# Kernel optimization log

Hardware: AMD Instinct MI355X
Metric: run time of the kernel (lower is better)

The kernel has to match this reference:

```python
import jax, jax.numpy as jnp
import numpy as np

EMBED_DIM = 1024
NUM_HEADS = 16
HEAD_DIM = EMBED_DIM // NUM_HEADS
TGT_LEN = 1024
SRC_LEN = 1024
BSZ = 4


def setup_inputs() -> dict:
    key = jax.random.key(0)
    ks = jax.random.split(key, 7)
    query = jax.random.normal(ks[0], (TGT_LEN, BSZ, EMBED_DIM), dtype=jnp.float32)
    key_t = jax.random.normal(ks[1], (SRC_LEN, BSZ, EMBED_DIM), dtype=jnp.float32)
    # hard 0/1 multiplicative mask applied post-softmax
    hard_attention = jax.random.randint(ks[2], (BSZ, TGT_LEN, SRC_LEN), 0, 2).astype(jnp.float32)
    # xavier_uniform_ on [3E, E]
    limit = float(np.sqrt(6.0 / (3 * EMBED_DIM + EMBED_DIM)))
    in_proj_weight = jax.random.uniform(ks[3], (3 * EMBED_DIM, EMBED_DIM), dtype=jnp.float32,
                                        minval=-limit, maxval=limit)
    in_proj_bias = jnp.zeros((3 * EMBED_DIM,), dtype=jnp.float32)
    limit_o = float(np.sqrt(1.0 / EMBED_DIM))
    out_proj_weight = jax.random.uniform(ks[4], (EMBED_DIM, EMBED_DIM), dtype=jnp.float32,
                                         minval=-limit_o, maxval=limit_o)
    out_proj_bias = jnp.zeros((EMBED_DIM,), dtype=jnp.float32)
    return {
        "query": query,
        "key": key_t,
        "hard_attention": hard_attention,
        "in_proj_weight": in_proj_weight,
        "in_proj_bias": in_proj_bias,
        "out_proj_weight": out_proj_weight,
        "out_proj_bias": out_proj_bias,
    }


def reference(query, key, hard_attention, in_proj_weight, in_proj_bias,
              out_proj_weight, out_proj_bias):
    tgt_len, bsz, embed_dim = query.shape
    src_len = key.shape[0]
    h, hd = NUM_HEADS, embed_dim // NUM_HEADS
    scaling = float(hd) ** -0.5

    # QKV projections (F.linear uses y = x @ W.T + b)
    wq = in_proj_weight[:embed_dim]
    wkv = in_proj_weight[embed_dim:]
    bq = in_proj_bias[:embed_dim]
    bkv = in_proj_bias[embed_dim:]
    q = jnp.einsum('tbe,fe->tbf', query, wq) + bq          # [T,B,E]
    kv = jnp.einsum('sbe,fe->sbf', key, wkv) + bkv          # [S,B,2E]
    k, v = jnp.split(kv, 2, axis=-1)

    q = (q * scaling).reshape(tgt_len, bsz, h, hd).transpose(1, 2, 0, 3)  # [B,H,T,D]
    k = k.reshape(src_len, bsz, h, hd).transpose(1, 2, 0, 3)              # [B,H,S,D]
    v = v.reshape(src_len, bsz, h, hd).transpose(1, 2, 0, 3)              # [B,H,S,D]

    scores = jnp.einsum('bhtd,bhsd->bhts', q, k)            # [B,H,T,S]
    attn = jax.nn.softmax(scores, axis=-1)
    # dropout_p = 0.0 -> identity
    attn = attn * hard_attention[:, None, :, :]             # post-softmax hard mask

    out = jnp.einsum('bhts,bhsd->bhtd', attn, v)            # [B,H,T,D]
    out = out.transpose(2, 0, 1, 3).reshape(tgt_len, bsz, embed_dim)
    out = jnp.einsum('tbe,fe->tbf', out, out_proj_weight) + out_proj_bias

    avg_weights = attn.sum(axis=1) / h                      # [B,T,S]
    return (out, avg_weights)
```

## Files before the change

### kernel.cpp

```cpp
#include <hip/hip_runtime.h>
#include <cstdint>
#include <cstddef>

typedef __bf16 bf16x8 __attribute__((ext_vector_type(8)));
typedef float  f32x4  __attribute__((ext_vector_type(4)));
typedef unsigned short u16x8 __attribute__((ext_vector_type(8)));

__device__ __forceinline__ uint16_t f2bf(float f) {
  uint32_t u = __float_as_uint(f);
  u += 0x7fffu + ((u >> 16) & 1u);
  return (uint16_t)(u >> 16);
}
__device__ __forceinline__ float bf2f(uint16_t u) {
  return __uint_as_float((uint32_t)u << 16);
}
__device__ __forceinline__ uint32_t cvtpk(float lo, float hi) {
  uint32_t r;
  asm("v_cvt_pk_bf16_f32 %0, %1, %2" : "=v"(r) : "v"(lo), "v"(hi));
  return r;
}

__device__ __forceinline__ f32x4 mfma16(bf16x8 a, bf16x8 b, f32x4 c) {
  return __builtin_amdgcn_mfma_f32_16x16x32_bf16(a, b, c, 0, 0, 0);
}

#define GLD_TO_LDS16(gptr, lptr)                                                   \
  __builtin_amdgcn_global_load_lds(                                                \
      (const __attribute__((address_space(1))) void*)(gptr),                       \
      (__attribute__((address_space(3))) void*)(lptr), 16, 0, 0)

__global__ void cvt_all(const float* __restrict__ q, const float* __restrict__ k,
                        const float* __restrict__ w, const float* __restrict__ wo,
                        uint16_t* __restrict__ Xq, uint16_t* __restrict__ Xk,
                        uint16_t* __restrict__ Wb, uint16_t* __restrict__ Wob) {
  int i = blockIdx.x * blockDim.x + threadIdx.x;
  const float* src;
  uint16_t* dst;
  int off;
  if (i < 1048576)      { src = q;  dst = Xq;  off = i; }
  else if (i < 2097152) { src = k;  dst = Xk;  off = i - 1048576; }
  else if (i < 2883584) { src = w;  dst = Wb;  off = i - 2097152; }
  else                  { src = wo; dst = Wob; off = i - 2883584; }
  float4 v = ((const float4*)src)[off];
  ushort4 o;
  o.x = f2bf(v.x); o.y = f2bf(v.y); o.z = f2bf(v.z); o.w = f2bf(v.w);
  ((ushort4*)dst)[off] = o;
}

__global__ void bitpack(const float* __restrict__ hard, uint32_t* __restrict__ bits) {
  int i = blockIdx.x * 256 + threadIdx.x;
  unsigned long long m = __ballot(hard[i] != 0.0f);
  if ((threadIdx.x & 63) == 0) {
    int w = i >> 5;
    bits[w]     = (uint32_t)m;
    bits[w + 1] = (uint32_t)(m >> 32);
  }
}

__global__ __launch_bounds__(512, 2)
void gemm_qkv8(const uint16_t* __restrict__ Xq, const uint16_t* __restrict__ Xk,
               const uint16_t* __restrict__ Wb, const float* __restrict__ ipb,
               uint16_t* __restrict__ Qb, uint16_t* __restrict__ Kb,
               uint16_t* __restrict__ Vt) {
  __shared__ __align__(16) char lds[131072];
  char* const Ab0 = lds;
  char* const Ab1 = lds + 32768;
  char* const Bb0 = lds + 65536;
  char* const Bb1 = lds + 98304;

  const int tid  = threadIdx.x;
  const int wave = tid >> 6, lane = tid & 63;
  const int quad = lane >> 4, l16 = lane & 15;
  const int wr = wave >> 2, wc = wave & 3;
  const int sw = (l16 & 7) << 4;

  const int swz = (blockIdx.x & 7) * 24 + (blockIdx.x >> 3);
  const uint16_t *Ag, *Bg;
  const float* bias;
  int bm, bn, mode;
  if (swz < 64) { mode = 0; Ag = Xq; Bg = Wb;            bias = ipb;        bm = swz >> 2; bn = swz & 3; }
  else { int u = swz - 64;
         mode = 1; Ag = Xk; Bg = Wb + (1 << 20); bias = ipb + 1024; bm = u >> 3;  bn = u & 7; }

  const char* Agb = (const char*)Ag + (size_t)bm * 256 * 2048;
  const char* Bgb = (const char*)Bg + (size_t)bn * 256 * 2048;

  const int lrow = lane >> 3;
  const size_t laneoff = (size_t)(wave * 8 + lrow) * 2048 + (((lane & 7) ^ lrow) << 4);

  auto stage = [&](const char* gb, char* lb, int hr, int tk) {
    GLD_TO_LDS16(gb + (size_t)hr * 131072 + (size_t)tk * 128 + laneoff,
                 lb + hr * 8192 + wave * 1024);
  };

  f32x4 acc[8][4] = {};
  bf16x8 a[4][2], b[2][2][2];

  auto rdA = [&](const char* Ac, int mh) {
#pragma unroll
    for (int mi = 0; mi < 4; mi++) {
      const char* p = Ac + (wr * 128 + mh * 64 + mi * 16 + l16) * 128;
#pragma unroll
      for (int ks = 0; ks < 2; ks++)
        a[mi][ks] = *(const bf16x8*)(p + ((ks * 64 + quad * 16) ^ sw));
    }
  };
  auto rdB = [&](const char* Bc, int nh) {
#pragma unroll
    for (int nj = 0; nj < 2; nj++) {
      const char* p = Bc + (wc * 64 + nh * 32 + nj * 16 + l16) * 128;
#pragma unroll
      for (int ks = 0; ks < 2; ks++)
        b[nh][nj][ks] = *(const bf16x8*)(p + ((ks * 64 + quad * 16) ^ sw));
    }
  };
  auto mm = [&](int mh, int nh) {
    __builtin_amdgcn_s_setprio(1);
#pragma unroll
    for (int ks = 0; ks < 2; ks++)
#pragma unroll
      for (int mi = 0; mi < 4; mi++)
#pragma unroll
        for (int nj = 0; nj < 2; nj++)
          acc[mh * 4 + mi][nh * 2 + nj] =
              mfma16(a[mi][ks], b[nh][nj][ks], acc[mh * 4 + mi][nh * 2 + nj]);
    __builtin_amdgcn_s_setprio(0);
  };

  auto ktile = [&](const char* Ac, const char* Bc, char* An, char* Bn,
                   int tn, bool pf) {
    rdA(Ac, 0); rdB(Bc, 0);
    if (pf) { stage(Agb, An, 0, tn); stage(Agb, An, 1, tn); stage(Agb, An, 2, tn); }
    __builtin_amdgcn_s_barrier();
    mm(0, 0);
    __builtin_amdgcn_s_barrier();
    rdB(Bc, 1);
    if (pf) { stage(Agb, An, 3, tn); stage(Bgb, Bn, 0, tn); stage(Bgb, Bn, 1, tn); }
    __builtin_amdgcn_s_barrier();
    mm(0, 1);
    __builtin_amdgcn_s_barrier();
    rdA(Ac, 1);
    if (pf) { stage(Bgb, Bn, 2, tn); stage(Bgb, Bn, 3, tn); }
    __builtin_amdgcn_s_barrier();
    mm(1, 0);
    __builtin_amdgcn_s_barrier();
    mm(1, 1);
    asm volatile("s_waitcnt vmcnt(0)" ::: "memory");
    __builtin_amdgcn_s_barrier();
  };

#pragma unroll
  for (int hr = 0; hr < 4; hr++) stage(Agb, Ab0, hr, 0);
#pragma unroll
  for (int hr = 0; hr < 4; hr++) stage(Bgb, Bb0, hr, 0);
  asm volatile("s_waitcnt vmcnt(0)" ::: "memory");
  __builtin_amdgcn_s_barrier();

  for (int tt = 0; tt < 16; tt += 2) {
    ktile(Ab0, Bb0, Ab1, Bb1, tt + 1, true);
    ktile(Ab1, Bb1, Ab0, Bb0, tt + 2, tt + 2 < 16);
  }

#pragma unroll
  for (int mi = 0; mi < 8; mi++)
#pragma unroll
    for (int j = 0; j < 4; j++)
#pragma unroll
      for (int r = 0; r < 4; r++) {
        int grow = bm * 256 + wr * 128 + mi * 16 + quad * 4 + r;
        int gf   = bn * 256 + wc * 64 + j * 16 + l16;
        float c = acc[mi][j][r] + bias[gf];
        if (mode == 0) {
          c *= 0.125f;
          int tq = grow >> 2, bb = grow & 3, h = gf >> 6, d = gf & 63;
          Qb[((((size_t)bb * 16 + h) << 10) + tq) * 64 + d] = f2bf(c);
        } else {
          int s = grow >> 2, bb = grow & 3;
          if (gf < 1024) {
            int h = gf >> 6, d = gf & 63;
            Kb[((((size_t)bb * 16 + h) << 10) + s) * 64 + d] = f2bf(c);
          } else {
            int fv = gf - 1024, h = fv >> 6, d = fv & 63;
            Vt[((((size_t)bb * 16 + h) * 64 + d) << 10) + s] = f2bf(c);
          }
        }
      }
}

__global__ __launch_bounds__(256)
void gemm_out(const uint16_t* __restrict__ A, const uint16_t* __restrict__ B,
              const float* __restrict__ bias, float* __restrict__ o32) {
  __shared__ __align__(16) uint16_t As[64 * 32];
  __shared__ __align__(16) uint16_t Bs[128 * 32];
  const int tid  = threadIdx.x;
  const int wave = tid >> 6, lane = tid & 63;
  const int quad = lane >> 4, l16 = lane & 15;
  const int bm = blockIdx.x >> 3, bn = blockIdx.x & 7;
  const int wm = (wave >> 1) << 5, wn = (wave & 1) << 6;
  const int K = 1024;

  f32x4 acc[2][4] = {};

  for (int k0 = 0; k0 < K; k0 += 32) {
    __syncthreads();
    {
      int c   = wave * 64 + lane;
      int row = c >> 2, kc = c & 3;
      const uint16_t* ga = A + (size_t)(bm * 64 + row) * K + k0 + kc * 8;
      GLD_TO_LDS16(ga, As + (size_t)(wave * 64) * 8);
    }
#pragma unroll
    for (int j = 0; j < 2; j++) {
      int c   = wave * 128 + j * 64 + lane;
      int row = c >> 2, kc = c & 3;
      const uint16_t* gb = B + (size_t)(bn * 128 + row) * K + k0 + kc * 8;
      GLD_TO_LDS16(gb, Bs + (size_t)(wave * 128 + j * 64) * 8);
    }
    __syncthreads();

    bf16x8 af[2], bfr[4];
#pragma unroll
    for (int i = 0; i < 2; i++)
      af[i] = *(const bf16x8*)(As + (wm + i * 16 + l16) * 32 + quad * 8);
#pragma unroll
    for (int i = 0; i < 4; i++)
      bfr[i] = *(const bf16x8*)(Bs + (wn + i * 16 + l16) * 32 + quad * 8);
#pragma unroll
    for (int mi = 0; mi < 2; mi++)
#pragma unroll
      for (int ni = 0; ni < 4; ni++)
        acc[mi][ni] = mfma16(af[mi], bfr[ni], acc[mi][ni]);
  }

#pragma unroll
  for (int mi = 0; mi < 2; mi++)
#pragma unroll
    for (int ni = 0; ni < 4; ni++)
#pragma unroll
      for (int r = 0; r < 4; r++) {
        int gi = bm * 64 + wm + mi * 16 + quad * 4 + r;
        int gf = bn * 128 + wn + ni * 16 + l16;
        o32[(size_t)gi * 1024 + gf] = acc[mi][ni][r] + bias[gf];
      }
}

__global__ __launch_bounds__(256, 2)
void attn_kernel(const uint16_t* __restrict__ qb, const uint16_t* __restrict__ kb,
                 const uint16_t* __restrict__ vtb, const uint32_t* __restrict__ bits,
                 uint16_t* __restrict__ attn_out, float* __restrict__ rlout) {
  __shared__ __align__(16) uint16_t Ks[128 * 64];
  __shared__ __align__(16) uint16_t Vs[64 * 128];
  __shared__ __align__(16) uint16_t Pb[4 * 32 * 128];

  const int bid = blockIdx.x;
  const int xcd = bid & 7, j = bid >> 3;
  const int slab = xcd * 8 + (j >> 3);
  const int b = slab >> 4, h = slab & 15;
  const int t0 = (j & 7) << 7;
  const int tid = threadIdx.x, wave = tid >> 6, lane = tid & 63;
  const int quad = lane >> 4, l16 = lane & 15;
  const int sw = (l16 & 7) << 4;
  const size_t bh = (size_t)b * 16 + h;
  const int tw = t0 + wave * 32;
  const int ta = tw + l16, tb = ta + 16;
  char* PwA = (char*)(Pb + wave * (32 * 128)) + l16 * 256;
  char* PwB = PwA + 16 * 256;

  const uint16_t* qA = qb + ((bh << 10) + ta) * 64;
  bf16x8 aqA0 = *(const bf16x8*)(qA + quad * 8);
  bf16x8 aqA1 = *(const bf16x8*)(qA + 32 + quad * 8);
  bf16x8 aqB0 = *(const bf16x8*)(qA + 1024 + quad * 8);
  bf16x8 aqB1 = *(const bf16x8*)(qA + 1024 + 32 + quad * 8);

  f32x4 accA[4] = {}, accB[4] = {};
  float smA = 0.f, smB = 0.f;

  const int kr = tid >> 3, kc8 = tid & 7;
  const int vr = tid >> 4, vc16 = tid & 15;

  const uint32_t* bA = bits + (((size_t)(b << 10) + ta) << 5);
  const uint32_t* bB = bits + (((size_t)(b << 10) + tb) << 5);

  u16x8 kreg[4], vreg[4];
#pragma unroll
  for (int r = 0; r < 4; r++)
    kreg[r] = *(const u16x8*)(kb + (bh << 16) + (size_t)(r * 256 + tid) * 8);
#pragma unroll
  for (int r = 0; r < 4; r++)
    vreg[r] = *(const u16x8*)(vtb + (((bh << 6) + r * 16 + vr) << 10) + vc16 * 8);
  uint4 uA = *(const uint4*)bA;
  uint4 uB = *(const uint4*)bB;

  for (int sc = 0; sc < 8; sc++) {
    uint32_t wA[4] = {uA.x >> (quad * 4), uA.y >> (quad * 4),
                      uA.z >> (quad * 4), uA.w >> (quad * 4)};
    uint32_t wB[4] = {uB.x >> (quad * 4), uB.y >> (quad * 4),
                      uB.z >> (quad * 4), uB.w >> (quad * 4)};

    __syncthreads();
#pragma unroll
    for (int r = 0; r < 4; r++) {
      const int row = r * 32 + kr;
      *(u16x8*)((char*)Ks + row * 128 + ((kc8 * 16) ^ ((row & 7) << 4))) = kreg[r];
    }
#pragma unroll
    for (int r = 0; r < 4; r++) {
      const int row = r * 16 + vr;
      *(u16x8*)((char*)Vs + row * 256 + ((vc16 * 16) ^ ((row & 7) << 4))) = vreg[r];
    }
    __syncthreads();

    if (sc < 7) {
      const uint16_t* kbase = kb + (bh << 16) + (size_t)(sc + 1) * 8192;
#pragma unroll
      for (int r = 0; r < 4; r++)
        kreg[r] = *(const u16x8*)(kbase + (size_t)(r * 256 + tid) * 8);
#pragma unroll
      for (int r = 0; r < 4; r++)
        vreg[r] = *(const u16x8*)(vtb + (((bh << 6) + r * 16 + vr) << 10) +
                                  (sc + 1) * 128 + vc16 * 8);
      uA = *(const uint4*)(bA + (sc + 1) * 4);
      uB = *(const uint4*)(bB + (sc + 1) * 4);
    }

#pragma unroll
    for (int nn = 0; nn < 8; nn++) {
      const char* kbp = (const char*)Ks + (nn * 16 + l16) * 128;
      bf16x8 bk0 = *(const bf16x8*)(kbp + ((quad * 16) ^ sw));
      bf16x8 bk1 = *(const bf16x8*)(kbp + ((64 + quad * 16) ^ sw));
      f32x4 cA = {}, cB = {};
      cA = mfma16(bk0, aqA0, cA); cA = mfma16(bk1, aqA1, cA);
      cB = mfma16(bk0, aqB0, cB); cB = mfma16(bk1, aqB1, cB);
      const uint32_t mA = wA[nn >> 1] >> ((nn & 1) * 16);
      const uint32_t mB = wB[nn >> 1] >> ((nn & 1) * 16);
      float eA[4], eB[4];
#pragma unroll
      for (int r = 0; r < 4; r++) {
        eA[r] = __expf(cA[r]); smA += eA[r];
        eB[r] = __expf(cB[r]); smB += eB[r];
        eA[r] = ((mA >> r) & 1) ? eA[r] : 0.f;
        eB[r] = ((mB >> r) & 1) ? eB[r] : 0.f;
      }
      const int pc = (nn * 32 + quad * 8) ^ sw;
      *(uint2*)(PwA + pc) = make_uint2(cvtpk(eA[0], eA[1]), cvtpk(eA[2], eA[3]));
      *(uint2*)(PwB + pc) = make_uint2(cvtpk(eB[0], eB[1]), cvtpk(eB[2], eB[3]));
    }

#pragma unroll
    for (int kc = 0; kc < 4; kc++) {
      const int pcb = (kc * 64 + quad * 16) ^ sw;
      bf16x8 apA = *(const bf16x8*)(PwA + pcb);
      bf16x8 apB = *(const bf16x8*)(PwB + pcb);
#pragma unroll
      for (int dt = 0; dt < 4; dt++) {
        bf16x8 bv = *(const bf16x8*)((const char*)Vs + (dt * 16 + l16) * 256 +
                                     ((kc * 64 + quad * 16) ^ sw));
        accA[dt] = mfma16(bv, apA, accA[dt]);
        accB[dt] = mfma16(bv, apB, accB[dt]);
      }
    }
  }

  smA += __shfl_xor(smA, 16); smA += __shfl_xor(smA, 32);
  smB += __shfl_xor(smB, 16); smB += __shfl_xor(smB, 32);
  const float rlA = 1.0f / smA, rlB = 1.0f / smB;
  if (quad == 0) rlout[(bh << 10) + ta] = rlA;
  if (quad == 1) rlout[(bh << 10) + tb] = rlB;

#pragma unroll
  for (int dt = 0; dt < 4; dt++) {
    uint2 oA = make_uint2(cvtpk(accA[dt][0] * rlA, accA[dt][1] * rlA),
                          cvtpk(accA[dt][2] * rlA, accA[dt][3] * rlA));
    *(uint2*)(attn_out + ((size_t)(ta * 4 + b) << 10) + h * 64 + dt * 16 + quad * 4) = oA;
    uint2 oB = make_uint2(cvtpk(accB[dt][0] * rlB, accB[dt][1] * rlB),
                          cvtpk(accB[dt][2] * rlB, accB[dt][3] * rlB));
    *(uint2*)(attn_out + ((size_t)(tb * 4 + b) << 10) + h * 64 + dt * 16 + quad * 4) = oB;
  }
}

__global__ __launch_bounds__(256, 2)
void avg_kernel(const uint16_t* __restrict__ qb, const uint16_t* __restrict__ kb,
                const float* __restrict__ rlin, const uint32_t* __restrict__ bits,
                float* __restrict__ avgout) {
  __shared__ __align__(16) uint16_t Ks[128 * 64];

  const int bid = blockIdx.x;
  const int xcd = bid & 7, j = bid >> 3;
  const int b  = xcd >> 1;
  const int t0 = ((xcd & 1) * 8 + (j >> 3)) << 6;
  const int s0 = (j & 7) << 7;
  const int tid = threadIdx.x, wave = tid >> 6, lane = tid & 63;
  const int quad = lane >> 4, l16 = lane & 15;
  const int sw = (l16 & 7) << 4;
  const int tr = t0 + wave * 16 + l16;
  const int kr = tid >> 3, kc8 = tid & 7;

  uint4 u = *(const uint4*)(bits + (((size_t)(b << 10) + tr) << 5) + (s0 >> 5));
  uint32_t w4[4] = {u.x >> (quad * 4), u.y >> (quad * 4),
                    u.z >> (quad * 4), u.w >> (quad * 4)};

  float av[8][4] = {};

  u16x8 kreg[4];
  {
    const uint16_t* kb0 = kb + ((((size_t)b * 16) << 10) + s0) * 64;
#pragma unroll
    for (int r = 0; r < 4; r++)
      kreg[r] = *(const u16x8*)(kb0 + (size_t)(r * 256 + tid) * 8);
  }

  for (int hh = 0; hh < 16; hh++) {
    __syncthreads();
#pragma unroll
    for (int r = 0; r < 4; r++) {
      const int row = r * 32 + kr;
      *(u16x8*)((char*)Ks + row * 128 + ((kc8 * 16) ^ ((row & 7) << 4))) = kreg[r];
    }
    __syncthreads();
    if (hh < 15) {
      const uint16_t* kb2 = kb + ((((size_t)b * 16 + hh + 1) << 10) + s0) * 64;
#pragma unroll
      for (int r = 0; r < 4; r++)
        kreg[r] = *(const u16x8*)(kb2 + (size_t)(r * 256 + tid) * 8);
    }

    const size_t bh = (size_t)b * 16 + hh;
    const uint16_t* qrow = qb + ((bh << 10) + tr) * 64;
    bf16x8 aq0 = *(const bf16x8*)(qrow + quad * 8);
    bf16x8 aq1 = *(const bf16x8*)(qrow + 32 + quad * 8);
    const float rl = rlin[(bh << 10) + tr];

#pragma unroll
    for (int n = 0; n < 8; n++) {
      const char* kbp = (const char*)Ks + (n * 16 + l16) * 128;
      bf16x8 bk0 = *(const bf16x8*)(kbp + ((quad * 16) ^ sw));
      bf16x8 bk1 = *(const bf16x8*)(kbp + ((64 + quad * 16) ^ sw));
      f32x4 c = {};
      c = mfma16(bk0, aq0, c);
      c = mfma16(bk1, aq1, c);
#pragma unroll
      for (int r = 0; r < 4; r++) av[n][r] += __expf(c[r]) * rl;
    }
  }

  float* orow = avgout + ((size_t)(b << 10) + tr) * 1024 + s0 + quad * 4;
#pragma unroll
  for (int n = 0; n < 8; n++) {
    const uint32_t m = w4[n >> 1] >> ((n & 1) * 16);
    float4 f;
    f.x = av[n][0] * (((m >> 0) & 1) ? 0.0625f : 0.f);
    f.y = av[n][1] * (((m >> 1) & 1) ? 0.0625f : 0.f);
    f.z = av[n][2] * (((m >> 2) & 1) ? 0.0625f : 0.f);
    f.w = av[n][3] * (((m >> 3) & 1) ? 0.0625f : 0.f);
    *(float4*)(orow + n * 16) = f;
  }
}

extern "C" void kernel_launch(void* const* d_in, const int* in_sizes, int n_in,
                              void* d_out, int out_size, void* d_ws, size_t ws_size,
                              hipStream_t stream) {
  const float* query = (const float*)d_in[0];
  const float* key   = (const float*)d_in[1];
  const float* hard  = (const float*)d_in[2];
  const float* ipw   = (const float*)d_in[3];
  const float* ipb   = (const float*)d_in[4];
  const float* opw   = (const float*)d_in[5];
  const float* opb   = (const float*)d_in[6];

  char* ws = (char*)d_ws;
  const size_t MB = 1ull << 20;
  uint16_t* Xq  = (uint16_t*)(ws + 0);
  uint16_t* Xk  = (uint16_t*)(ws + 8 * MB);
  uint16_t* Wb  = (uint16_t*)(ws + 16 * MB);
  uint16_t* Wob = (uint16_t*)(ws + 22 * MB);
  uint16_t* Qb  = (uint16_t*)(ws + 24 * MB);
  uint16_t* Kb  = (uint16_t*)(ws + 32 * MB);
  uint16_t* Vt  = (uint16_t*)(ws + 40 * MB);
  uint16_t* AO  = Xq;

  float* out = (float*)d_out;
  float* avg = out + 4194304;
  uint32_t* bits  = (uint32_t*)out;
  float*    rlbuf = out + 131072;

  cvt_all<<<12288, 256, 0, stream>>>(query, key, ipw, opw, Xq, Xk, Wb, Wob);
  bitpack<<<16384, 256, 0, stream>>>(hard, bits);

  gemm_qkv8<<<192, 512, 0, stream>>>(Xq, Xk, Wb, ipb, Qb, Kb, Vt);

  attn_kernel<<<512, 256, 0, stream>>>(Qb, Kb, Vt, bits, AO, rlbuf);

  avg_kernel<<<512, 256, 0, stream>>>(Qb, Kb, rlbuf, bits, avg);

  gemm_out<<<512, 256, 0, stream>>>(AO, Wob, opb, out);
}
```

Before: 251.8 us.

## Double-buffer MFMA operand registers to prefetch next k-tile fragments

Splits the A/B register fragments into two sets so the next k-tile's first fragments are read from LDS before the final MFMA block of the current tile, and regroups the global-to-LDS staging into fewer phases. The aim is to hide LDS read latency behind MFMA work across the k-tile boundary. It raises register pressure, which may cut occupancy or cause spills, and it changes barrier placement.

```diff
diff --git a/kernel.cpp b/kernel.cpp
--- a/kernel.cpp
+++ b/kernel.cpp
@@ -94,9 +94,9 @@
   };
 
   f32x4 acc[8][4] = {};
-  bf16x8 a[4][2], b[2][2][2];
-
-  auto rdA = [&](const char* Ac, int mh) {
+  bf16x8 a0[4][2], a1[4][2], b0[2][2], b1[2][2];
+
+  auto rdA = [&](const char* Ac, int mh, bf16x8 (&a)[4][2]) {
 #pragma unroll
     for (int mi = 0; mi < 4; mi++) {
       const char* p = Ac + (wr * 128 + mh * 64 + mi * 16 + l16) * 128;
@@ -105,16 +105,16 @@
         a[mi][ks] = *(const bf16x8*)(p + ((ks * 64 + quad * 16) ^ sw));
     }
   };
-  auto rdB = [&](const char* Bc, int nh) {
+  auto rdB = [&](const char* Bc, int nh, bf16x8 (&b)[2][2]) {
 #pragma unroll
     for (int nj = 0; nj < 2; nj++) {
       const char* p = Bc + (wc * 64 + nh * 32 + nj * 16 + l16) * 128;
 #pragma unroll
       for (int ks = 0; ks < 2; ks++)
-        b[nh][nj][ks] = *(const bf16x8*)(p + ((ks * 64 + quad * 16) ^ sw));
+        b[nj][ks] = *(const bf16x8*)(p + ((ks * 64 + quad * 16) ^ sw));
     }
   };
-  auto mm = [&](int mh, int nh) {
+  auto mm = [&](int mh, int nh, bf16x8 (&a)[4][2], bf16x8 (&b)[2][2]) {
     __builtin_amdgcn_s_setprio(1);
 #pragma unroll
     for (int ks = 0; ks < 2; ks++)
@@ -123,29 +123,29 @@
 #pragma unroll
         for (int nj = 0; nj < 2; nj++)
           acc[mh * 4 + mi][nh * 2 + nj] =
-              mfma16(a[mi][ks], b[nh][nj][ks], acc[mh * 4 + mi][nh * 2 + nj]);
+              mfma16(a[mi][ks], b[nj][ks], acc[mh * 4 + mi][nh * 2 + nj]);
     __builtin_amdgcn_s_setprio(0);
   };
 
   auto ktile = [&](const char* Ac, const char* Bc, char* An, char* Bn,
                    int tn, bool pf) {
-    rdA(Ac, 0); rdB(Bc, 0);
+    rdB(Bc, 1, b1);
     if (pf) { stage(Agb, An, 0, tn); stage(Agb, An, 1, tn); stage(Agb, An, 2, tn); }
     __builtin_amdgcn_s_barrier();
-    mm(0, 0);
-    __builtin_amdgcn_s_barrier();
-    rdB(Bc, 1);
-    if (pf) { stage(Agb, An, 3, tn); stage(Bgb, Bn, 0, tn); stage(Bgb, Bn, 1, tn); }
-    __builtin_amdgcn_s_barrier();
-    mm(0, 1);
-    __builtin_amdgcn_s_barrier();
-    rdA(Ac, 1);
-    if (pf) { stage(Bgb, Bn, 2, tn); stage(Bgb, Bn, 3, tn); }
-    __builtin_amdgcn_s_barrier();
-    mm(1, 0);
-    __builtin_amdgcn_s_barrier();
-    mm(1, 1);
+    mm(0, 0, a0, b0);
+    __builtin_amdgcn_s_barrier();
+    rdA(Ac, 1, a1);
+    if (pf) { stage(Agb, An, 3, tn); stage(Bgb, Bn, 0, tn); stage(Bgb, Bn, 1, tn);
+              stage(Bgb, Bn, 2, tn); stage(Bgb, Bn, 3, tn); }
+    __builtin_amdgcn_s_barrier();
+    mm(0, 1, a0, b1);
+    __builtin_amdgcn_s_barrier();
+    mm(1, 0, a1, b0);
     asm volatile("s_waitcnt vmcnt(0)" ::: "memory");
+    __builtin_amdgcn_s_barrier();
+    if (pf) { rdA(An, 0, a0); rdB(Bn, 0, b0); }
+    __builtin_amdgcn_s_barrier();
+    mm(1, 1, a1, b1);
     __builtin_amdgcn_s_barrier();
   };
 
@@ -155,6 +155,7 @@
   for (int hr = 0; hr < 4; hr++) stage(Bgb, Bb0, hr, 0);
   asm volatile("s_waitcnt vmcnt(0)" ::: "memory");
   __builtin_amdgcn_s_barrier();
+  rdA(Ab0, 0, a0); rdB(Bb0, 0, b0);
 
   for (int tt = 0; tt < 16; tt += 2) {
     ktile(Ab0, Bb0, Ab1, Bb1, tt + 1, true);
```

Result: slower. 267.2 us (+6.1%).
